# Kernel optimization log

Hardware: AMD Instinct MI355X
Metric: run time of the kernel (lower is better)

Reference implementation:

```python
import jax, jax.numpy as jnp
import numpy as np

TEMPERATURE = 0.5
NEG_INF_FILL = -1000000000.0


def setup_inputs() -> dict:
    key = jax.random.key(0)
    z = jax.random.normal(key, (16384, 128), dtype=jnp.float32)
    # module expects L2-normalized projected features
    z = z / jnp.linalg.norm(z, axis=-1, keepdims=True)
    return {"z": z}


def reference(z) -> jnp.ndarray:
    N2 = z.shape[0]
    N = N2 // 2
    # (2N, 2N) pairwise similarity scaled by temperature
    sim = (z @ z.T) / TEMPERATURE
    # mask self-similarity on the diagonal
    eye = jnp.eye(N2, dtype=bool)
    sim = jnp.where(eye, NEG_INF_FILL, sim)
    # positive pair index: row i < N pairs with i+N; row i >= N pairs with i-N
    pos_idx = jnp.concatenate([jnp.arange(N, N2), jnp.arange(0, N)])
    positives = sim[jnp.arange(N2), pos_idx]
    loss = -positives + jax.scipy.special.logsumexp(sim, axis=1)
    return loss.mean()
```

## Files before the change

### kernel.cpp

```cpp
#include <hip/hip_runtime.h>
#include <hip/hip_bf16.h>

#define N2    16384
#define NHALF 8192
#define KDIM  128
#define WCOLS 32
#define BCOLS 128
#define NHCOL 8192
#define NITER (NHCOL / BCOLS)

using bf16x8 = __attribute__((ext_vector_type(8))) short;
using f32x4  = __attribute__((ext_vector_type(4))) float;

#if __has_builtin(__builtin_amdgcn_exp2f)
#define EXP2F(x) __builtin_amdgcn_exp2f(x)
#else
#define EXP2F(x) exp2f(x)
#endif
#if __has_builtin(__builtin_amdgcn_logf)
#define LOG2F(x) __builtin_amdgcn_logf(x)
#else
#define LOG2F(x) log2f(x)
#endif

#define PRESCALE 1.6986436005760381f

typedef const __attribute__((address_space(1))) void* gas_ptr;
typedef __attribute__((address_space(3))) void* las_ptr;

__device__ __forceinline__ unsigned short f2bf(float f) {
  unsigned u = __float_as_uint(f);
  u += 0x7fffu + ((u >> 16) & 1u);
  return (unsigned short)(u >> 16);
}

__global__ void k_convert(const float* __restrict__ z, unsigned short* __restrict__ zb,
                          float* __restrict__ S, float* __restrict__ out) {
  int i = blockIdx.x * blockDim.x + threadIdx.x;
  if (i < N2) S[i] = 0.f;
  if (i == 0) out[0] = 0.f;
  float4 v = reinterpret_cast<const float4*>(z)[i];
  ushort4 o;
  o.x = f2bf(v.x * PRESCALE); o.y = f2bf(v.y * PRESCALE);
  o.z = f2bf(v.z * PRESCALE); o.w = f2bf(v.w * PRESCALE);
  reinterpret_cast<ushort4*>(zb)[i] = o;
}

__global__ __launch_bounds__(256, 2) void k_main(const unsigned short* __restrict__ zb,
                                                 float* __restrict__ S) {
  __shared__ __align__(16) unsigned short Bs[4][2][WCOLS * KDIM];
  const int t    = threadIdx.x;
  const int w    = t >> 6;
  const int l    = t & 63;
  const int q    = l >> 4;
  const int c15  = l & 15;
  const int rg   = blockIdx.x >> 1;
  const int half = blockIdx.x & 1;
  const int rbase = rg * 64;

  int srcoff[8];
#pragma unroll
  for (int j = 0; j < 8; ++j) {
    int p   = j * 64 + l;
    int row = p >> 4;
    int pg  = p & 15;
    int k8  = pg ^ (row & 15);
    srcoff[j] = (row * 16 + k8) * 16;
  }

  const char* sbase = (const char*)zb + (size_t)(half * NHCOL + w * WCOLS) * KDIM * 2;

#pragma unroll
  for (int j = 0; j < 8; ++j)
    __builtin_amdgcn_global_load_lds((gas_ptr)(sbase + srcoff[j]),
                                     (las_ptr)(&Bs[w][0][j * 512]), 16, 0, 0);

  bf16x8 afr[4][4];
#pragma unroll
  for (int m = 0; m < 4; ++m) {
    const unsigned short* ap = zb + (size_t)(rbase + m * 16 + c15) * KDIM + q * 8;
#pragma unroll
    for (int s = 0; s < 4; ++s)
      afr[m][s] = *reinterpret_cast<const bf16x8*>(ap + s * 32);
  }
#pragma unroll
  for (int m = 0; m < 4; ++m)
#pragma unroll
    for (int s = 0; s < 4; ++s)
      asm volatile("" : "+v"(afr[m][s]));

  float rowsum[4][4];
#pragma unroll
  for (int m = 0; m < 4; ++m)
#pragma unroll
    for (int r = 0; r < 4; ++r) rowsum[m][r] = 0.f;

  const int dOff0 = (half * NHCOL + w * WCOLS) - rbase;

  for (int it = 0; it < NITER; ++it) {
    const int buf = it & 1;
    if (it + 1 < NITER) {
      const char* src = sbase + (size_t)(it + 1) * BCOLS * KDIM * 2;
#pragma unroll
      for (int j = 0; j < 8; ++j)
        __builtin_amdgcn_global_load_lds((gas_ptr)(src + srcoff[j]),
                                         (las_ptr)(&Bs[w][buf ^ 1][j * 512]), 16, 0, 0);
      asm volatile("s_waitcnt vmcnt(8)" ::: "memory");
    } else {
      asm volatile("s_waitcnt vmcnt(0)" ::: "memory");
    }

    bf16x8 bfr[4][2];
#pragma unroll
    for (int s = 0; s < 4; ++s)
#pragma unroll
      for (int n = 0; n < 2; ++n) {
        int idx = (n * 16 + c15) * KDIM + (((s * 4 + q) ^ c15) * 8);
        bfr[s][n] = *reinterpret_cast<const bf16x8*>(&Bs[w][buf][idx]);
      }

    f32x4 acc[4][2];
#pragma unroll
    for (int m = 0; m < 4; ++m)
#pragma unroll
      for (int n = 0; n < 2; ++n) acc[m][n] = (f32x4){0.f, 0.f, 0.f, 0.f};
#pragma unroll
    for (int s = 0; s < 4; ++s)
#pragma unroll
      for (int m = 0; m < 4; ++m)
#pragma unroll
        for (int n = 0; n < 2; ++n)
          acc[m][n] = __builtin_amdgcn_mfma_f32_16x16x32_bf16(afr[m][s], bfr[s][n],
                                                              acc[m][n], 0, 0, 0);

    const int dOff = dOff0 + it * BCOLS;
#pragma unroll
    for (int m = 0; m < 4; ++m)
#pragma unroll
      for (int n = 0; n < 2; ++n) {
        const bool dfrag = (dOff == (m - n) * 16);
#pragma unroll
        for (int r = 0; r < 4; ++r) {
          float e = EXP2F(acc[m][n][r]);
          if (dfrag && (c15 == q * 4 + r)) e = 0.f;
          rowsum[m][r] += e;
        }
      }
  }

#pragma unroll
  for (int m = 0; m < 4; ++m)
#pragma unroll
    for (int r = 0; r < 4; ++r) {
      float v = rowsum[m][r];
      v += __shfl_xor(v, 1);
      v += __shfl_xor(v, 2);
      v += __shfl_xor(v, 4);
      v += __shfl_xor(v, 8);
      if (c15 == 0) atomicAdd(&S[rbase + m * 16 + q * 4 + r], v);
    }
}

__global__ void k_final(const float* __restrict__ z, const float* __restrict__ S,
                        float* __restrict__ out) {
  __shared__ float red[256];
  int t = threadIdx.x;
  int i = blockIdx.x * 256 + t;
  int j = i ^ NHALF;
  const float4* zi = reinterpret_cast<const float4*>(z + (size_t)i * KDIM);
  const float4* zj = reinterpret_cast<const float4*>(z + (size_t)j * KDIM);
  float dot = 0.f;
#pragma unroll
  for (int k = 0; k < KDIM / 4; ++k) {
    float4 a = zi[k], b = zj[k];
    dot += a.x * b.x + a.y * b.y + a.z * b.z + a.w * b.w;
  }
  float loss = LOG2F(S[i]) * 0.69314718055994531f - 2.f * dot;
  red[t] = loss;
  __syncthreads();
  for (int o = 128; o > 0; o >>= 1) {
    if (t < o) red[t] += red[t + o];
    __syncthreads();
  }
  if (t == 0) atomicAdd(out, red[0] * (1.f / N2));
}

extern "C" void kernel_launch(void* const* d_in, const int* in_sizes, int n_in,
                              void* d_out, int out_size, void* d_ws, size_t ws_size,
                              hipStream_t stream) {
  const float* z = (const float*)d_in[0];
  float* out = (float*)d_out;
  unsigned short* zb = (unsigned short*)d_ws;
  float* S = (float*)((char*)d_ws + (size_t)N2 * KDIM * 2);

  k_convert<<<(N2 * KDIM / 4) / 256, 256, 0, stream>>>(z, zb, S, out);
  k_main<<<(N2 / 64) * 2, 256, 0, stream>>>(zb, S);
  k_final<<<N2 / 256, 256, 0, stream>>>(z, S, out);
}
```

Baseline: 146.2 us.

## Software-pipeline MFMA and exp epilogue with double accumulators and sched barriers

Splits the main loop into two accumulator sets so the MFMA matmul for the next tile is issued while the exp2/rowsum epilogue of the previous tile runs. The loop is manually unrolled by two, and sched_group_barrier hints interleave one MFMA with three VALU ops. The goal is to hide the transcendental epilogue behind matrix-core work. The cost is a second 32-register accumulator set, which raises VGPR pressure at 2 waves per SIMD and could cause spills.

```diff
diff --git a/kernel.cpp b/kernel.cpp
--- a/kernel.cpp
+++ b/kernel.cpp
@@ -97,56 +97,93 @@
 
   const int dOff0 = (half * NHCOL + w * WCOLS) - rbase;
 
-  for (int it = 0; it < NITER; ++it) {
-    const int buf = it & 1;
-    if (it + 1 < NITER) {
-      const char* src = sbase + (size_t)(it + 1) * BCOLS * KDIM * 2;
-#pragma unroll
-      for (int j = 0; j < 8; ++j)
-        __builtin_amdgcn_global_load_lds((gas_ptr)(src + srcoff[j]),
-                                         (las_ptr)(&Bs[w][buf ^ 1][j * 512]), 16, 0, 0);
-      asm volatile("s_waitcnt vmcnt(8)" ::: "memory");
-    } else {
-      asm volatile("s_waitcnt vmcnt(0)" ::: "memory");
-    }
-
-    bf16x8 bfr[4][2];
-#pragma unroll
-    for (int s = 0; s < 4; ++s)
-#pragma unroll
-      for (int n = 0; n < 2; ++n) {
-        int idx = (n * 16 + c15) * KDIM + (((s * 4 + q) ^ c15) * 8);
-        bfr[s][n] = *reinterpret_cast<const bf16x8*>(&Bs[w][buf][idx]);
-      }
-
-    f32x4 acc[4][2];
-#pragma unroll
-    for (int m = 0; m < 4; ++m)
-#pragma unroll
-      for (int n = 0; n < 2; ++n) acc[m][n] = (f32x4){0.f, 0.f, 0.f, 0.f};
-#pragma unroll
-    for (int s = 0; s < 4; ++s)
-#pragma unroll
-      for (int m = 0; m < 4; ++m)
-#pragma unroll
-        for (int n = 0; n < 2; ++n)
-          acc[m][n] = __builtin_amdgcn_mfma_f32_16x16x32_bf16(afr[m][s], bfr[s][n],
-                                                              acc[m][n], 0, 0, 0);
-
-    const int dOff = dOff0 + it * BCOLS;
-#pragma unroll
-    for (int m = 0; m < 4; ++m)
-#pragma unroll
-      for (int n = 0; n < 2; ++n) {
-        const bool dfrag = (dOff == (m - n) * 16);
-#pragma unroll
-        for (int r = 0; r < 4; ++r) {
-          float e = EXP2F(acc[m][n][r]);
-          if (dfrag && (c15 == q * 4 + r)) e = 0.f;
-          rowsum[m][r] += e;
-        }
-      }
-  }
+  f32x4 accA[4][2], accB[4][2];
+
+#define STAGE_BODY(T, CB, NB, ACC, PREFETCH, VMCNT_ASM)                        \
+  {                                                                            \
+    if (PREFETCH) {                                                            \
+      const char* _src = sbase + (size_t)((T) + 1) * BCOLS * KDIM * 2;         \
+      _Pragma("unroll")                                                        \
+      for (int j = 0; j < 8; ++j)                                              \
+        __builtin_amdgcn_global_load_lds((gas_ptr)(_src + srcoff[j]),          \
+                                         (las_ptr)(&Bs[w][NB][j * 512]), 16, 0, 0); \
+    }                                                                          \
+    asm volatile(VMCNT_ASM ::: "memory");                                      \
+    bf16x8 bfr[4][2];                                                          \
+    _Pragma("unroll")                                                          \
+    for (int s = 0; s < 4; ++s)                                                \
+      _Pragma("unroll")                                                        \
+      for (int n = 0; n < 2; ++n) {                                            \
+        int idx = (n * 16 + c15) * KDIM + (((s * 4 + q) ^ c15) * 8);           \
+        bfr[s][n] = *reinterpret_cast<const bf16x8*>(&Bs[w][CB][idx]);         \
+      }                                                                        \
+    _Pragma("unroll")                                                          \
+    for (int m = 0; m < 4; ++m)                                                \
+      _Pragma("unroll")                                                        \
+      for (int n = 0; n < 2; ++n)                                              \
+        ACC[m][n] = __builtin_amdgcn_mfma_f32_16x16x32_bf16(                   \
+            afr[m][0], bfr[0][n], (f32x4){0.f, 0.f, 0.f, 0.f}, 0, 0, 0);       \
+    _Pragma("unroll")                                                          \
+    for (int s = 1; s < 4; ++s)                                                \
+      _Pragma("unroll")                                                        \
+      for (int m = 0; m < 4; ++m)                                              \
+        _Pragma("unroll")                                                      \
+        for (int n = 0; n < 2; ++n)                                            \
+          ACC[m][n] = __builtin_amdgcn_mfma_f32_16x16x32_bf16(                 \
+              afr[m][s], bfr[s][n], ACC[m][n], 0, 0, 0);                       \
+  }
+
+#define STAGE_P(T, CB, NB, ACC) STAGE_BODY(T, CB, NB, ACC, 1, "s_waitcnt vmcnt(8)")
+#define STAGE_L(T, CB, ACC)     STAGE_BODY(T, CB, 0,  ACC, 0, "s_waitcnt vmcnt(0)")
+
+#define EPI(ACC, IT)                                                           \
+  {                                                                            \
+    const int _dOff = dOff0 + (IT) * BCOLS;                                    \
+    _Pragma("unroll")                                                          \
+    for (int m = 0; m < 4; ++m)                                                \
+      _Pragma("unroll")                                                        \
+      for (int n = 0; n < 2; ++n) {                                            \
+        const bool dfrag = (_dOff == (m - n) * 16);                            \
+        _Pragma("unroll")                                                      \
+        for (int r = 0; r < 4; ++r) {                                          \
+          float e = EXP2F(ACC[m][n][r]);                                       \
+          if (dfrag && (c15 == q * 4 + r)) e = 0.f;                            \
+          rowsum[m][r] += e;                                                   \
+        }                                                                      \
+      }                                                                        \
+  }
+
+#define SGB_INTERLEAVE                                                         \
+  {                                                                            \
+    __builtin_amdgcn_sched_group_barrier(0x100, 8, 0);          \
+    _Pragma("unroll")                                                          \
+    for (int u = 0; u < 32; ++u) {                                             \
+      __builtin_amdgcn_sched_group_barrier(0x008, 1, 0);          \
+      __builtin_amdgcn_sched_group_barrier(0x002, 3, 0);          \
+    }                                                                          \
+  }
+
+  STAGE_P(0, 0, 1, accA);
+#pragma unroll 1
+  for (int p = 0; p < NITER / 2 - 1; ++p) {
+    const int it = 2 * p;
+    STAGE_P(it + 1, 1, 0, accB);
+    EPI(accA, it);
+    SGB_INTERLEAVE;
+    STAGE_P(it + 2, 0, 1, accA);
+    EPI(accB, it + 1);
+    SGB_INTERLEAVE;
+  }
+  STAGE_L(NITER - 1, 1, accB);
+  EPI(accA, NITER - 2);
+  SGB_INTERLEAVE;
+  EPI(accB, NITER - 1);
+
+#undef STAGE_BODY
+#undef STAGE_P
+#undef STAGE_L
+#undef EPI
+#undef SGB_INTERLEAVE
 
 #pragma unroll
   for (int m = 0; m < 4; ++m)
```

Measured after the change: 144.5 us. About the same (-1.2%).
